# Kernel optimization log

Hardware: AMD Instinct MI355X
Metric: run time of the kernel (lower is better)

Reference implementation:

```python
import jax, jax.numpy as jnp
import numpy as np

# Problem sizes: batch B, n variables, m constraints (dense nnz pattern)
B, N, M = 256, 128, 192
# OSQP ADMM parameters (scaling=0, fixed rho; OSQP defaults)
RHO = 0.1      # step size
SIGMA = 1e-6   # regularization
ALPHA = 1.6    # relaxation
N_ITERS = 400  # fixed iteration count (jit-friendly surrogate for max_iter/tolerances)


def setup_inputs() -> dict:
    key = jax.random.key(0)
    k1, k2, k3, k4, k5, k6 = jax.random.split(key, 6)
    G = jax.random.normal(k1, (B, N, N), dtype=jnp.float32)
    # PSD quadratic cost: P = G G^T / n + 0.5 I
    P_val = jnp.einsum('bij,bkj->bik', G, G) / N + 0.5 * jnp.eye(N, dtype=jnp.float32)
    q_val = jax.random.normal(k2, (B, N), dtype=jnp.float32)
    A_val = jax.random.normal(k3, (B, M, N), dtype=jnp.float32) / jnp.sqrt(jnp.float32(N))
    # Bounds bracketing a feasible point x0 so every QP is solvable
    x0 = jax.random.normal(k4, (B, N), dtype=jnp.float32)
    z0 = jnp.einsum('bmn,bn->bm', A_val, x0)
    l_val = z0 - jnp.abs(jax.random.normal(k5, (B, M), dtype=jnp.float32)) - 0.1
    u_val = z0 + jnp.abs(jax.random.normal(k6, (B, M), dtype=jnp.float32)) + 0.1
    return {'P_val': P_val, 'q_val': q_val, 'A_val': A_val,
            'l_val': l_val, 'u_val': u_val}


def _osqp_admm(P, q, A, l, u):
    """Batched OSQP ADMM with fixed rho: solves argmin 1/2 x'Px + q'x s.t. l<=Ax<=u."""
    dt = P.dtype
    I_n = jnp.eye(N, dtype=dt)
    I_m = jnp.eye(M, dtype=dt)
    AT = jnp.swapaxes(A, -1, -2)  # [B, n, m]
    # KKT matrix [[P + sigma*I, A'], [A, -I/rho]]  -> [B, n+m, n+m]
    top = jnp.concatenate([P + SIGMA * I_n, AT], axis=-1)
    bot = jnp.concatenate([A, jnp.broadcast_to(-(1.0 / RHO) * I_m, (P.shape[0], M, M))], axis=-1)
    K = jnp.concatenate([top, bot], axis=-2)
    Kinv = jnp.linalg.inv(K)  # factorize once (rho fixed)

    x0 = jnp.zeros_like(q)
    z0 = jnp.zeros_like(l)
    y0 = jnp.zeros_like(l)

    def step(carry, _):
        x, z, y = carry
        rhs = jnp.concatenate([SIGMA * x - q, z - y / RHO], axis=-1)  # [B, n+m]
        sol = jnp.einsum('bij,bj->bi', Kinv, rhs)
        xt, nu = sol[:, :N], sol[:, N:]
        zt = z + (nu - y) / RHO
        x_new = ALPHA * xt + (1.0 - ALPHA) * x
        zc = ALPHA * zt + (1.0 - ALPHA) * z
        z_new = jnp.clip(zc + y / RHO, l, u)  # projection onto [l, u]
        y_new = y + RHO * (zc - z_new)
        return (x_new, z_new, y_new), None

    (x, z, y), _ = jax.lax.scan(step, (x0, z0, y0), None, length=N_ITERS)
    return x


def reference(P_val, q_val, A_val, l_val, u_val):
    # Returns the batch of primal solutions x_hat, shape [B, n]
    return _osqp_admm(P_val, q_val, A_val, l_val, u_val)
```

## Files before the change

kernel.cpp:

```cpp
#include <hip/hip_runtime.h>


#define Nn 128
#define Mm 192
constexpr float RHO_    = 0.1f;
constexpr float RHOINV_ = 10.0f;
constexpr float SIGMA_  = 1e-6f;
constexpr float ALPHA_  = 1.6f;
constexpr int   NITERS_ = 400;

typedef float v2f __attribute__((ext_vector_type(2)));
typedef float v4f __attribute__((ext_vector_type(4)));

template<int CTRL>
__device__ __forceinline__ float dpp_add(float x) {
  int y = __builtin_amdgcn_update_dpp(__float_as_int(x), __float_as_int(x),
                                      CTRL, 0xF, 0xF, false);
  return x + __int_as_float(y);
}
__device__ __forceinline__ float red16(float x) {
  x = dpp_add<0x121>(x); x = dpp_add<0x122>(x);
  x = dpp_add<0x124>(x); x = dpp_add<0x128>(x);
  return x;
}

template<int K0>
__device__ __forceinline__ void gj_block(float rr[32], float* __restrict__ buf0,
                                         float* __restrict__ buf1,
                                         const int irow, const int qq) {
  const bool qsel = (qq == K0);
  #pragma unroll
  for (int kk = 0; kk < 32; kk++) {
    const int k = 32*K0 + kk;
    float* wb = ((kk & 1) == 0) ? buf0 : buf1;
    if (irow == k) {
      #pragma unroll
      for (int j4 = 0; j4 < 8; j4++)
        *(float4*)&wb[36*qq + 4*j4] = *(const float4*)&rr[4*j4];
    }
    __syncthreads();
    const float akk  = wb[36*K0 + kk];
    float pinv = __builtin_amdgcn_rcpf(akk);
    pinv = pinv + pinv*(1.0f - akk*pinv);
    constexpr int QP = K0 | (K0<<2) | (K0<<4) | (K0<<6);
    const int fi = __builtin_amdgcn_update_dpp(__float_as_int(rr[kk]),
                      __float_as_int(rr[kk]), QP, 0xF, 0xF, false);
    const float f = __int_as_float(fi);
    const bool piv = (irow == k);
    float gfac = f * pinv;
    gfac = piv ? (1.0f - pinv) : gfac;
    float rk[32];
    #pragma unroll
    for (int j4 = 0; j4 < 8; j4++)
      *(float4*)&rk[4*j4] = *(const float4*)&wb[36*qq + 4*j4];
    #pragma unroll
    for (int j = 0; j < 32; j++) rr[j] -= gfac * rk[j];
    const float pivfix = piv ? pinv : -gfac;
    if (qsel) rr[kk] = pivfix;
  }
}

__global__ void __launch_bounds__(512, 2)
precompute_kernel(const float* __restrict__ Pg, const float* __restrict__ qg,
                  const float* __restrict__ Ag, float* __restrict__ wsWt,
                  float* __restrict__ wsC)
{
  __shared__ float smem[16384];
  const int t = threadIdx.x;
  const int b = blockIdx.x;
  const float* __restrict__ Pb = Pg + (size_t)b*Nn*Nn;
  const float* __restrict__ qb = qg + (size_t)b*Nn;
  const float* __restrict__ Ab = Ag + (size_t)b*Mm*Nn;

  {
    const int ar = t & 31;
    const int bc = t >> 5;
    float acc[4][8];
    #pragma unroll
    for (int a=0;a<4;a++)
      #pragma unroll
      for (int j=0;j<8;j++) acc[a][j]=0.f;

    for (int c=0;c<6;c++) {
      __syncthreads();
      {
        const float4* src = (const float4*)(Ab + c*32*Nn);
        float4* dst = (float4*)smem;
        dst[t]     = src[t];
        dst[t+512] = src[t+512];
      }
      __syncthreads();
      #pragma unroll 2
      for (int m=0;m<32;m++) {
        const float4 ra  = *(const float4*)&smem[m*Nn + 4*ar];
        const float4 cb0 = *(const float4*)&smem[m*Nn + 8*bc];
        const float4 cb1 = *(const float4*)&smem[m*Nn + 8*bc + 4];
        const float rv[4] = {ra.x, ra.y, ra.z, ra.w};
        const float cv[8] = {cb0.x,cb0.y,cb0.z,cb0.w,cb1.x,cb1.y,cb1.z,cb1.w};
        #pragma unroll
        for (int a=0;a<4;a++)
          #pragma unroll
          for (int j=0;j<8;j++) acc[a][j] += rv[a]*cv[j];
      }
    }
    __syncthreads();
    #pragma unroll
    for (int a=0;a<4;a++) {
      const int i = 4*ar + a;
      #pragma unroll
      for (int j=0;j<8;j++) {
        const int jj = 8*bc + j;
        float v = Pb[i*Nn + jj] + RHO_*acc[a][j];
        if (i == jj) v += SIGMA_;
        smem[i*Nn + jj] = v;
      }
    }
    __syncthreads();
  }

  {
    const int irow = t >> 2;
    const int qq   = t & 3;
    float rr[32];
    #pragma unroll
    for (int j=0;j<32;j++) rr[j] = smem[irow*Nn + 32*qq + j];
    __syncthreads();
    float* buf0 = smem;
    float* buf1 = smem + 144;
    gj_block<0>(rr, buf0, buf1, irow, qq);
    gj_block<1>(rr, buf0, buf1, irow, qq);
    gj_block<2>(rr, buf0, buf1, irow, qq);
    gj_block<3>(rr, buf0, buf1, irow, qq);
    __syncthreads();
    #pragma unroll
    for (int j=0;j<32;j++) smem[irow*Nn + 32*qq + j] = rr[j];
  }
  __syncthreads();

  {
    const int jr = t & 63, kc = t >> 6;
    v2f acc[3][8];
    #pragma unroll
    for (int a=0;a<3;a++)
      #pragma unroll
      for (int p=0;p<8;p++) acc[a][p] = (v2f){0.f,0.f};

    for (int mi=0; mi<32; mi++) {
      const v4f a0 = *(const v4f*)&Ab[(jr      )*Nn + 4*mi];
      const v4f a1 = *(const v4f*)&Ab[(jr +  64)*Nn + 4*mi];
      const v4f a2 = *(const v4f*)&Ab[(jr + 128)*Nn + 4*mi];
      const float am[3][4] = {{a0.x,a0.y,a0.z,a0.w},
                              {a1.x,a1.y,a1.z,a1.w},
                              {a2.x,a2.y,a2.z,a2.w}};
      #pragma unroll
      for (int q=0;q<4;q++) {
        const int m = 4*mi + q;
        const v4f w0 = *(const v4f*)&smem[m*Nn + 16*kc +  0];
        const v4f w1 = *(const v4f*)&smem[m*Nn + 16*kc +  4];
        const v4f w2 = *(const v4f*)&smem[m*Nn + 16*kc +  8];
        const v4f w3 = *(const v4f*)&smem[m*Nn + 16*kc + 12];
        const v2f wp[8] = {(v2f){w0.x,w0.y},(v2f){w0.z,w0.w},
                           (v2f){w1.x,w1.y},(v2f){w1.z,w1.w},
                           (v2f){w2.x,w2.y},(v2f){w2.z,w2.w},
                           (v2f){w3.x,w3.y},(v2f){w3.z,w3.w}};
        #pragma unroll
        for (int a=0;a<3;a++) {
          const v2f amv = (v2f){am[a][q], am[a][q]};
          #pragma unroll
          for (int p=0;p<8;p++) acc[a][p] += amv * wp[p];
        }
      }
    }
    float* wb = wsWt + (size_t)b*Mm*Nn;
    #pragma unroll
    for (int a=0;a<3;a++) {
      const int j = jr + 64*a;
      #pragma unroll
      for (int x=0;x<4;x++) {
        *(float4*)&wb[j*Nn + 16*kc + 4*x] =
          make_float4(acc[a][2*x].x, acc[a][2*x].y, acc[a][2*x+1].x, acc[a][2*x+1].y);
      }
    }
  }
  if (t < Nn) {
    float cc = 0.f;
    #pragma unroll 4
    for (int k=0;k<Nn;k++) cc += smem[k*Nn + t] * qb[k];
    wsC[(size_t)b*Nn + t] = cc;
  }
}

#define ABASE 0
#define WBASE 6912
__global__ void __launch_bounds__(1024, 4)
loop_kernel(const float* __restrict__ Ag, const float* __restrict__ lg,
            const float* __restrict__ ug, const float* __restrict__ wsWt,
            const float* __restrict__ wsC, float* __restrict__ outg)
{
  __shared__ float smem[13824];
  const int t = threadIdx.x, b = blockIdx.x;
  const int ig = t >> 4, cg = t & 15;
  const float* __restrict__ Ab = Ag   + (size_t)b*Mm*Nn;
  const float* __restrict__ Wb = wsWt + (size_t)b*Mm*Nn;
  const float* __restrict__ cb = wsC  + (size_t)b*Nn;

  const int  pm  = 64*cg + ig;
  const bool isp = (cg < 3);

  float dreg = 0.f, lreg = 0.f, ureg = 0.f;
  if (isp) {
    lreg = lg[(size_t)b*Mm + pm];
    ureg = ug[(size_t)b*Mm + pm];
    const float4* ar = (const float4*)(Ab + pm*Nn);
    const float4* cr = (const float4*)cb;
    #pragma unroll 4
    for (int k4=0;k4<32;k4++) {
      const float4 av = ar[k4], cv = cr[k4];
      dreg += av.x*cv.x + av.y*cv.y + av.z*cv.z + av.w*cv.w;
    }
  }

  v2f accv[3][12];
  #pragma unroll
  for (int a=0;a<3;a++)
    #pragma unroll
    for (int jj=0;jj<12;jj++) accv[a][jj] = (v2f){0.f,0.f};

  for (int kc=0; kc<4; kc++) {
    __syncthreads();
    {
      int x = t;
      {
        const int row = x>>3, c4 = x&7;
        *(float4*)&smem[ABASE + 36*row + 4*c4] = *(const float4*)&Ab[row*Nn + 32*kc + 4*c4];
        *(float4*)&smem[WBASE + 36*row + 4*c4] = *(const float4*)&Wb[row*Nn + 32*kc + 4*c4];
      }
      if (t < 512) {
        x = t + 1024;
        const int row = x>>3, c4 = x&7;
        *(float4*)&smem[ABASE + 36*row + 4*c4] = *(const float4*)&Ab[row*Nn + 32*kc + 4*c4];
        *(float4*)&smem[WBASE + 36*row + 4*c4] = *(const float4*)&Wb[row*Nn + 32*kc + 4*c4];
      }
    }
    __syncthreads();
    #pragma unroll
    for (int m4=0; m4<8; m4++) {
      const v4f a0 = *(const v4f*)&smem[ABASE + 36*(ig      ) + 4*m4];
      const v4f a1 = *(const v4f*)&smem[ABASE + 36*(ig +  64) + 4*m4];
      const v4f a2 = *(const v4f*)&smem[ABASE + 36*(ig + 128) + 4*m4];
      #pragma unroll
      for (int jj=0; jj<12; jj++) {
        const v4f w = *(const v4f*)&smem[WBASE + 36*(cg + 16*jj) + 4*m4];
        const v2f wlo = (v2f){w.x,w.y}, whi = (v2f){w.z,w.w};
        accv[0][jj] += (v2f){a0.x,a0.y}*wlo + (v2f){a0.z,a0.w}*whi;
        accv[1][jj] += (v2f){a1.x,a1.y}*wlo + (v2f){a1.z,a1.w}*whi;
        accv[2][jj] += (v2f){a2.x,a2.y}*wlo + (v2f){a2.z,a2.w}*whi;
      }
    }
  }
  float Vr[3][12];
  #pragma unroll
  for (int a=0;a<3;a++)
    #pragma unroll
    for (int jj=0;jj<12;jj++)
      Vr[a][jj] = accv[a][jj].x + accv[a][jj].y;

  __syncthreads();
  float* sT0  = smem;
  float* sT1  = smem + 192;
  float* sacc = smem + 384;
  if (t < Mm) sT0[t] = 0.f;
  __syncthreads();

  const int woff = (pm & 15)*12 + (pm >> 4);
  float sreg = 0.f, preg = 0.f, Sacc = 0.f;
  const float* sR0 = sT0 + 12*cg;
  const float* sR1 = sT1 + 12*cg;

#define ITER(RD, WR)                                                           \
  {                                                                            \
    const float4 sA = *(const float4*)(RD);                                    \
    const float4 sB = *(const float4*)((RD) + 4);                              \
    const float4 sC = *(const float4*)((RD) + 8);                              \
    float r0 = Vr[0][0]*sA.x + Vr[0][1]*sA.y + Vr[0][2]*sA.z + Vr[0][3]*sA.w   \
             + Vr[0][4]*sB.x + Vr[0][5]*sB.y + Vr[0][6]*sB.z + Vr[0][7]*sB.w   \
             + Vr[0][8]*sC.x + Vr[0][9]*sC.y + Vr[0][10]*sC.z + Vr[0][11]*sC.w;\
    float r1 = Vr[1][0]*sA.x + Vr[1][1]*sA.y + Vr[1][2]*sA.z + Vr[1][3]*sA.w   \
             + Vr[1][4]*sB.x + Vr[1][5]*sB.y + Vr[1][6]*sB.z + Vr[1][7]*sB.w   \
             + Vr[1][8]*sC.x + Vr[1][9]*sC.y + Vr[1][10]*sC.z + Vr[1][11]*sC.w;\
    float r2 = Vr[2][0]*sA.x + Vr[2][1]*sA.y + Vr[2][2]*sA.z + Vr[2][3]*sA.w   \
             + Vr[2][4]*sB.x + Vr[2][5]*sB.y + Vr[2][6]*sB.z + Vr[2][7]*sB.w   \
             + Vr[2][8]*sC.x + Vr[2][9]*sC.y + Vr[2][10]*sC.z + Vr[2][11]*sC.w;\
    r0 = red16(r0); r1 = red16(r1); r2 = red16(r2);                            \
    if (isp) {                                                                 \
      const float r  = (cg==0) ? r0 : ((cg==1) ? r1 : r2);                     \
      const float w  = r - dreg;                                               \
      const float v  = fmaf(ALPHA_, w, preg);                                  \
      const float z  = __builtin_amdgcn_fmed3f(v, lreg, ureg);                 \
      const float sn = RHO_ * fmaf(2.0f, z, -v);                               \
      (WR)[woff] = sn;                                                         \
      Sacc = (1.f-ALPHA_)*Sacc + ALPHA_*sreg;                                  \
      sreg = sn;                                                               \
      preg = fmaf(-ALPHA_, z, v);                                              \
    }                                                                          \
    __syncthreads();                                                           \
  }

  #pragma unroll 1
  for (int it2 = 0; it2 < NITERS_/2; it2++) {
    ITER(sR0, sT1)
    ITER(sR1, sT0)
  }
#undef ITER

  if (isp) sacc[pm] = Sacc;
  __syncthreads();
  if (t < Nn) {
    float acc = -cb[t];
    #pragma unroll 4
    for (int j=0;j<Mm;j++) acc += Wb[j*Nn + t] * sacc[j];
    outg[(size_t)b*Nn + t] = acc;
  }
}

extern "C" void kernel_launch(void* const* d_in, const int* in_sizes, int n_in,
                              void* d_out, int out_size, void* d_ws, size_t ws_size,
                              hipStream_t stream) {
  const float* P = (const float*)d_in[0];
  const float* q = (const float*)d_in[1];
  const float* A = (const float*)d_in[2];
  const float* l = (const float*)d_in[3];
  const float* u = (const float*)d_in[4];
  (void)in_sizes; (void)n_in; (void)out_size; (void)ws_size;
  float* wsWt = (float*)d_ws;
  float* wsC  = wsWt + (size_t)256*Mm*Nn;
  precompute_kernel<<<256, 512, 0, stream>>>(P, q, A, wsWt, wsC);
  loop_kernel<<<256, 1024, 0, stream>>>(A, l, u, wsWt, wsC, (float*)d_out);
}
```

Before: 437.9 us.

## Double precompute block to 1024 threads with 8-way Gauss-Jordan row split

Precompute kernel now runs 1024 threads per block. Each Gauss-Jordan row is split across 8 lanes of 16 columns, using ds_swizzle to broadcast the pivot column, and the A^T A and W GEMM tiles are re-partitioned for the larger block. The loop kernel's initial V GEMM switches from packed v2f accumulation to scalar FMAs. This aims to raise parallelism and cut per-thread register pressure in the serial inversion, at the cost of more barrier participants and possibly more scalar instructions in the loop-kernel setup.

```diff
diff --git a/kernel.cpp b/kernel.cpp
--- a/kernel.cpp
+++ b/kernel.cpp
@@ -4,12 +4,10 @@
 #define Nn 128
 #define Mm 192
 constexpr float RHO_    = 0.1f;
-constexpr float RHOINV_ = 10.0f;
 constexpr float SIGMA_  = 1e-6f;
 constexpr float ALPHA_  = 1.6f;
 constexpr int   NITERS_ = 400;
 
-typedef float v2f __attribute__((ext_vector_type(2)));
 typedef float v4f __attribute__((ext_vector_type(4)));
 
 template<int CTRL>
@@ -25,42 +23,38 @@
 }
 
 template<int K0>
-__device__ __forceinline__ void gj_block(float rr[32], float* __restrict__ buf0,
-                                         float* __restrict__ buf1,
-                                         const int irow, const int qq) {
-  const bool qsel = (qq == K0);
+__device__ __forceinline__ void gj_block8(float rr[16], float* __restrict__ buf0,
+                                          float* __restrict__ buf1,
+                                          const int irow, const int oct) {
   #pragma unroll
-  for (int kk = 0; kk < 32; kk++) {
-    const int k = 32*K0 + kk;
+  for (int kk = 0; kk < 16; kk++) {
+    const int k = 16*K0 + kk;
     float* wb = ((kk & 1) == 0) ? buf0 : buf1;
     if (irow == k) {
       #pragma unroll
-      for (int j4 = 0; j4 < 8; j4++)
-        *(float4*)&wb[36*qq + 4*j4] = *(const float4*)&rr[4*j4];
-    }
-    __syncthreads();
-    const float akk  = wb[36*K0 + kk];
+      for (int j4 = 0; j4 < 4; j4++)
+        *(float4*)&wb[20*oct + 4*j4] = *(const float4*)&rr[4*j4];
+    }
+    __syncthreads();
+    const float akk = wb[20*K0 + kk];
     float pinv = __builtin_amdgcn_rcpf(akk);
     pinv = pinv + pinv*(1.0f - akk*pinv);
-    constexpr int QP = K0 | (K0<<2) | (K0<<4) | (K0<<6);
-    const int fi = __builtin_amdgcn_update_dpp(__float_as_int(rr[kk]),
-                      __float_as_int(rr[kk]), QP, 0xF, 0xF, false);
+    const int fi = __builtin_amdgcn_ds_swizzle(__float_as_int(rr[kk]),
+                                               (K0 << 5) | 0x18);
     const float f = __int_as_float(fi);
     const bool piv = (irow == k);
-    float gfac = f * pinv;
-    gfac = piv ? (1.0f - pinv) : gfac;
-    float rk[32];
-    #pragma unroll
-    for (int j4 = 0; j4 < 8; j4++)
-      *(float4*)&rk[4*j4] = *(const float4*)&wb[36*qq + 4*j4];
-    #pragma unroll
-    for (int j = 0; j < 32; j++) rr[j] -= gfac * rk[j];
-    const float pivfix = piv ? pinv : -gfac;
-    if (qsel) rr[kk] = pivfix;
-  }
-}
-
-__global__ void __launch_bounds__(512, 2)
+    const float gfac = piv ? (1.0f - pinv) : (f * pinv);
+    float rk[16];
+    #pragma unroll
+    for (int j4 = 0; j4 < 4; j4++)
+      *(float4*)&rk[4*j4] = *(const float4*)&wb[20*oct + 4*j4];
+    #pragma unroll
+    for (int j = 0; j < 16; j++) rr[j] -= gfac * rk[j];
+    if (oct == K0) rr[kk] = piv ? pinv : -gfac;
+  }
+}
+
+__global__ void __launch_bounds__(1024, 4)
 precompute_kernel(const float* __restrict__ Pg, const float* __restrict__ qg,
                   const float* __restrict__ Ag, float* __restrict__ wsWt,
                   float* __restrict__ wsC)
@@ -75,111 +69,104 @@
   {
     const int ar = t & 31;
     const int bc = t >> 5;
-    float acc[4][8];
+    float acc[4][4];
     #pragma unroll
     for (int a=0;a<4;a++)
       #pragma unroll
-      for (int j=0;j<8;j++) acc[a][j]=0.f;
+      for (int v=0;v<4;v++) acc[a][v]=0.f;
 
     for (int c=0;c<6;c++) {
       __syncthreads();
       {
-        const float4* src = (const float4*)(Ab + c*32*Nn);
-        float4* dst = (float4*)smem;
-        dst[t]     = src[t];
-        dst[t+512] = src[t+512];
+        ((float4*)smem)[t] = ((const float4*)(Ab + c*32*Nn))[t];
       }
       __syncthreads();
-      #pragma unroll 2
+      #pragma unroll 4
       for (int m=0;m<32;m++) {
-        const float4 ra  = *(const float4*)&smem[m*Nn + 4*ar];
-        const float4 cb0 = *(const float4*)&smem[m*Nn + 8*bc];
-        const float4 cb1 = *(const float4*)&smem[m*Nn + 8*bc + 4];
-        const float rv[4] = {ra.x, ra.y, ra.z, ra.w};
-        const float cv[8] = {cb0.x,cb0.y,cb0.z,cb0.w,cb1.x,cb1.y,cb1.z,cb1.w};
+        const float4 ri = *(const float4*)&smem[m*Nn + 4*ar];
+        const float4 rj = *(const float4*)&smem[m*Nn + 4*bc];
+        const float iv[4] = {ri.x,ri.y,ri.z,ri.w};
+        const float jv[4] = {rj.x,rj.y,rj.z,rj.w};
         #pragma unroll
         for (int a=0;a<4;a++)
           #pragma unroll
-          for (int j=0;j<8;j++) acc[a][j] += rv[a]*cv[j];
+          for (int v=0;v<4;v++) acc[a][v] += iv[a]*jv[v];
       }
     }
     __syncthreads();
     #pragma unroll
     for (int a=0;a<4;a++) {
       const int i = 4*ar + a;
-      #pragma unroll
-      for (int j=0;j<8;j++) {
-        const int jj = 8*bc + j;
-        float v = Pb[i*Nn + jj] + RHO_*acc[a][j];
-        if (i == jj) v += SIGMA_;
-        smem[i*Nn + jj] = v;
-      }
+      const float4 p = *(const float4*)&Pb[i*Nn + 4*bc];
+      float4 o;
+      o.x = p.x + RHO_*acc[a][0] + ((i==4*bc+0)?SIGMA_:0.f);
+      o.y = p.y + RHO_*acc[a][1] + ((i==4*bc+1)?SIGMA_:0.f);
+      o.z = p.z + RHO_*acc[a][2] + ((i==4*bc+2)?SIGMA_:0.f);
+      o.w = p.w + RHO_*acc[a][3] + ((i==4*bc+3)?SIGMA_:0.f);
+      *(float4*)&smem[i*Nn + 4*bc] = o;
     }
     __syncthreads();
   }
 
   {
-    const int irow = t >> 2;
-    const int qq   = t & 3;
-    float rr[32];
-    #pragma unroll
-    for (int j=0;j<32;j++) rr[j] = smem[irow*Nn + 32*qq + j];
+    const int irow = t >> 3;
+    const int oct  = t & 7;
+    float rr[16];
+    #pragma unroll
+    for (int j4=0;j4<4;j4++)
+      *(float4*)&rr[4*j4] = *(const float4*)&smem[irow*Nn + 16*oct + 4*j4];
     __syncthreads();
     float* buf0 = smem;
-    float* buf1 = smem + 144;
-    gj_block<0>(rr, buf0, buf1, irow, qq);
-    gj_block<1>(rr, buf0, buf1, irow, qq);
-    gj_block<2>(rr, buf0, buf1, irow, qq);
-    gj_block<3>(rr, buf0, buf1, irow, qq);
-    __syncthreads();
-    #pragma unroll
-    for (int j=0;j<32;j++) smem[irow*Nn + 32*qq + j] = rr[j];
+    float* buf1 = smem + 160;
+    gj_block8<0>(rr, buf0, buf1, irow, oct);
+    gj_block8<1>(rr, buf0, buf1, irow, oct);
+    gj_block8<2>(rr, buf0, buf1, irow, oct);
+    gj_block8<3>(rr, buf0, buf1, irow, oct);
+    gj_block8<4>(rr, buf0, buf1, irow, oct);
+    gj_block8<5>(rr, buf0, buf1, irow, oct);
+    gj_block8<6>(rr, buf0, buf1, irow, oct);
+    gj_block8<7>(rr, buf0, buf1, irow, oct);
+    __syncthreads();
+    #pragma unroll
+    for (int j4=0;j4<4;j4++)
+      *(float4*)&smem[irow*Nn + 16*oct + 4*j4] = *(const float4*)&rr[4*j4];
   }
   __syncthreads();
 
   {
-    const int jr = t & 63, kc = t >> 6;
-    v2f acc[3][8];
+    const int rg = t >> 4, cg = t & 15;
+    float acc[3][8];
     #pragma unroll
     for (int a=0;a<3;a++)
       #pragma unroll
-      for (int p=0;p<8;p++) acc[a][p] = (v2f){0.f,0.f};
-
-    for (int mi=0; mi<32; mi++) {
-      const v4f a0 = *(const v4f*)&Ab[(jr      )*Nn + 4*mi];
-      const v4f a1 = *(const v4f*)&Ab[(jr +  64)*Nn + 4*mi];
-      const v4f a2 = *(const v4f*)&Ab[(jr + 128)*Nn + 4*mi];
-      const float am[3][4] = {{a0.x,a0.y,a0.z,a0.w},
-                              {a1.x,a1.y,a1.z,a1.w},
-                              {a2.x,a2.y,a2.z,a2.w}};
+      for (int p=0;p<8;p++) acc[a][p]=0.f;
+
+    for (int k4=0;k4<32;k4++) {
+      v4f av[3];
+      av[0] = *(const v4f*)&Ab[(rg      )*Nn + 4*k4];
+      av[1] = *(const v4f*)&Ab[(rg +  64)*Nn + 4*k4];
+      av[2] = *(const v4f*)&Ab[(rg + 128)*Nn + 4*k4];
       #pragma unroll
       for (int q=0;q<4;q++) {
-        const int m = 4*mi + q;
-        const v4f w0 = *(const v4f*)&smem[m*Nn + 16*kc +  0];
-        const v4f w1 = *(const v4f*)&smem[m*Nn + 16*kc +  4];
-        const v4f w2 = *(const v4f*)&smem[m*Nn + 16*kc +  8];
-        const v4f w3 = *(const v4f*)&smem[m*Nn + 16*kc + 12];
-        const v2f wp[8] = {(v2f){w0.x,w0.y},(v2f){w0.z,w0.w},
-                           (v2f){w1.x,w1.y},(v2f){w1.z,w1.w},
-                           (v2f){w2.x,w2.y},(v2f){w2.z,w2.w},
-                           (v2f){w3.x,w3.y},(v2f){w3.z,w3.w}};
+        const int m = 4*k4 + q;
+        const v4f w0 = *(const v4f*)&smem[m*Nn + 8*cg];
+        const v4f w1 = *(const v4f*)&smem[m*Nn + 8*cg + 4];
         #pragma unroll
         for (int a=0;a<3;a++) {
-          const v2f amv = (v2f){am[a][q], am[a][q]};
-          #pragma unroll
-          for (int p=0;p<8;p++) acc[a][p] += amv * wp[p];
+          const float amq = (q==0)?av[a].x : (q==1)?av[a].y : (q==2)?av[a].z : av[a].w;
+          acc[a][0] += amq*w0.x; acc[a][1] += amq*w0.y;
+          acc[a][2] += amq*w0.z; acc[a][3] += amq*w0.w;
+          acc[a][4] += amq*w1.x; acc[a][5] += amq*w1.y;
+          acc[a][6] += amq*w1.z; acc[a][7] += amq*w1.w;
         }
       }
     }
     float* wb = wsWt + (size_t)b*Mm*Nn;
     #pragma unroll
     for (int a=0;a<3;a++) {
-      const int j = jr + 64*a;
-      #pragma unroll
-      for (int x=0;x<4;x++) {
-        *(float4*)&wb[j*Nn + 16*kc + 4*x] =
-          make_float4(acc[a][2*x].x, acc[a][2*x].y, acc[a][2*x+1].x, acc[a][2*x+1].y);
-      }
+      const int j = rg + 64*a;
+      *(float4*)&wb[j*Nn + 8*cg]     = make_float4(acc[a][0],acc[a][1],acc[a][2],acc[a][3]);
+      *(float4*)&wb[j*Nn + 8*cg + 4] = make_float4(acc[a][4],acc[a][5],acc[a][6],acc[a][7]);
     }
   }
   if (t < Nn) {
@@ -220,11 +207,11 @@
     }
   }
 
-  v2f accv[3][12];
+  float Vr[3][12];
   #pragma unroll
   for (int a=0;a<3;a++)
     #pragma unroll
-    for (int jj=0;jj<12;jj++) accv[a][jj] = (v2f){0.f,0.f};
+    for (int jj=0;jj<12;jj++) Vr[a][jj] = 0.f;
 
   for (int kc=0; kc<4; kc++) {
     __syncthreads();
@@ -251,19 +238,12 @@
       #pragma unroll
       for (int jj=0; jj<12; jj++) {
         const v4f w = *(const v4f*)&smem[WBASE + 36*(cg + 16*jj) + 4*m4];
-        const v2f wlo = (v2f){w.x,w.y}, whi = (v2f){w.z,w.w};
-        accv[0][jj] += (v2f){a0.x,a0.y}*wlo + (v2f){a0.z,a0.w}*whi;
-        accv[1][jj] += (v2f){a1.x,a1.y}*wlo + (v2f){a1.z,a1.w}*whi;
-        accv[2][jj] += (v2f){a2.x,a2.y}*wlo + (v2f){a2.z,a2.w}*whi;
-      }
-    }
-  }
-  float Vr[3][12];
-  #pragma unroll
-  for (int a=0;a<3;a++)
-    #pragma unroll
-    for (int jj=0;jj<12;jj++)
-      Vr[a][jj] = accv[a][jj].x + accv[a][jj].y;
+        Vr[0][jj] += a0.x*w.x + a0.y*w.y + a0.z*w.z + a0.w*w.w;
+        Vr[1][jj] += a1.x*w.x + a1.y*w.y + a1.z*w.z + a1.w*w.w;
+        Vr[2][jj] += a2.x*w.x + a2.y*w.y + a2.z*w.z + a2.w*w.w;
+      }
+    }
+  }
 
   __syncthreads();
   float* sT0  = smem;
@@ -334,6 +314,6 @@
   (void)in_sizes; (void)n_in; (void)out_size; (void)ws_size;
   float* wsWt = (float*)d_ws;
   float* wsC  = wsWt + (size_t)256*Mm*Nn;
-  precompute_kernel<<<256, 512, 0, stream>>>(P, q, A, wsWt, wsC);
+  precompute_kernel<<<256, 1024, 0, stream>>>(P, q, A, wsWt, wsC);
   loop_kernel<<<256, 1024, 0, stream>>>(A, l, u, wsWt, wsC, (float*)d_out);
 }
```

Result: slower. 909.5 us (+107.7%).
